# Kernel optimization log

Hardware: AMD Instinct MI355X
Metric: run time of the kernel (lower is better)

Reference implementation:

```python
import jax, jax.numpy as jnp
import numpy as np

B, S, D, H = 32, 577, 768, 12
d = D // H  # dim per head
MLP = 4 * D
EPS = 1e-5


def setup_inputs() -> dict:
    key = jax.random.key(0)
    ks = jax.random.split(key, 6)
    sc = 0.02
    return {
        "x": jax.random.normal(ks[0], (B, S, D), jnp.float32),
        "ln1_g": jnp.ones((D,), jnp.float32),
        "ln1_b": jnp.zeros((D,), jnp.float32),
        "Wq": jax.random.normal(ks[1], (H, d, d), jnp.float32) * sc,
        "bq": jnp.zeros((H, d), jnp.float32),
        "Wk": jax.random.normal(ks[2], (H, d, d), jnp.float32) * sc,
        "bk": jnp.zeros((H, d), jnp.float32),
        "Wv": jax.random.normal(ks[3], (H, d, d), jnp.float32) * sc,
        "bv": jnp.zeros((H, d), jnp.float32),
        "ln2_g": jnp.ones((D,), jnp.float32),
        "ln2_b": jnp.zeros((D,), jnp.float32),
        "W1": jax.random.normal(ks[4], (D, MLP), jnp.float32) * sc,
        "b1": jnp.zeros((MLP,), jnp.float32),
        "W2": jax.random.normal(ks[5], (MLP, D), jnp.float32) * sc,
        "b2": jnp.zeros((D,), jnp.float32),
    }


def layer_norm(x, g, b):
    mu = jnp.mean(x, axis=-1, keepdims=True)
    var = jnp.mean(jnp.square(x - mu), axis=-1, keepdims=True)
    return (x - mu) * jax.lax.rsqrt(var + EPS) * g + b


def msa(x, Wq, bq, Wk, bk, Wv, bv):
    # x: [B,S,D]; each head only sees its own slice of the hidden dim.
    xh = x.reshape(B, S, H, d)
    q = jnp.einsum("bshd,hde->bshe", xh, Wq) + bq
    k = jnp.einsum("bshd,hde->bshe", xh, Wk) + bk
    v = jnp.einsum("bshd,hde->bshe", xh, Wv) + bv
    scores = jnp.einsum("bqhe,bkhe->bhqk", q, k) / jnp.sqrt(jnp.float32(d))
    attn = jax.nn.softmax(scores, axis=-1)  # [B,H,S,S]
    out = jnp.einsum("bhqk,bkhe->bqhe", attn, v)
    return out.reshape(B, S, D)  # head-wise hstack == reshape


def reference(x, ln1_g, ln1_b, Wq, bq, Wk, bk, Wv, bv, ln2_g, ln2_b, W1, b1, W2, b2):
    out = x + msa(layer_norm(x, ln1_g, ln1_b), Wq, bq, Wk, bk, Wv, bv)
    h = layer_norm(out, ln2_g, ln2_b)
    mlp = jax.nn.gelu(h @ W1 + b1, approximate=False) @ W2 + b2
    return out + mlp
```

## Files before the change

kernel.cpp:

```cpp
#include <hip/hip_runtime.h>
#include <hip/hip_bf16.h>


#define kB   32
#define kS   577
#define kD   768
#define kH   12
#define kd   64
#define kMLP 3072
#define kTOK (kB * kS)
#define kMPAD 18688

typedef short short8 __attribute__((ext_vector_type(8)));
typedef short short4v __attribute__((ext_vector_type(4)));
typedef float f32x4 __attribute__((ext_vector_type(4)));
typedef float f32x16 __attribute__((ext_vector_type(16)));
typedef unsigned u32x4 __attribute__((ext_vector_type(4)));
typedef __bf16 bf16x8 __attribute__((ext_vector_type(8)));

__device__ inline short f2bf(float f) {
  unsigned u = __float_as_uint(f);
  unsigned r = (u + 0x7FFFu + ((u >> 16) & 1u)) >> 16;
  return (short)r;
}

__device__ inline f32x4 mfma16(short8 a, short8 b, f32x4 c) {
  return __builtin_amdgcn_mfma_f32_16x16x32_bf16(
      __builtin_bit_cast(bf16x8, a), __builtin_bit_cast(bf16x8, b), c, 0, 0, 0);
}

__device__ inline f32x16 mfma32(short8 a, short8 b, f32x16 c) {
  return __builtin_amdgcn_mfma_f32_32x32x16_bf16(
      __builtin_bit_cast(bf16x8, a), __builtin_bit_cast(bf16x8, b), c, 0, 0, 0);
}

__device__ inline void load_lds16(const short* g, short* l) {
  __builtin_amdgcn_global_load_lds(
      (__attribute__((address_space(1))) void*)(g),
      (__attribute__((address_space(3))) void*)(l), 16, 0, 0);
}

__device__ inline unsigned cvtpk(float lo, float hi) {
  unsigned r;
  asm("v_cvt_pk_bf16_f32 %0, %1, %2" : "=v"(r) : "v"(lo), "v"(hi));
  return r;
}

__device__ inline void pl32(unsigned &a, unsigned &b) {
  typedef int int2v __attribute__((ext_vector_type(2)));
  int2v r = __builtin_amdgcn_permlane32_swap((int)a, (int)b, false, false);
  a = (unsigned)r[0];
  b = (unsigned)r[1];
}

__device__ inline float gelu_f(float x) {
  float u = x * x;
  float z = x * fmaf(0.0713548162f, u, 1.5957691216f);
  float e = __expf(z);
  return x - x / (e + 1.0f);
}

__global__ __launch_bounds__(256) void ln_kernel(const float* __restrict__ x,
                                                 const float* __restrict__ g,
                                                 const float* __restrict__ b,
                                                 short* __restrict__ out) {
  int row = blockIdx.x;
  const float* xr = x + (size_t)row * kD;
  int t = threadIdx.x;
  float v0 = xr[t], v1 = xr[t + 256], v2 = xr[t + 512];
  float s = v0 + v1 + v2;
  float ss = v0 * v0 + v1 * v1 + v2 * v2;
#pragma unroll
  for (int off = 1; off < 64; off <<= 1) {
    s += __shfl_xor(s, off, 64);
    ss += __shfl_xor(ss, off, 64);
  }
  __shared__ float red[8];
  int wid = t >> 6;
  if ((t & 63) == 0) { red[wid * 2] = s; red[wid * 2 + 1] = ss; }
  __syncthreads();
  s = red[0] + red[2] + red[4] + red[6];
  ss = red[1] + red[3] + red[5] + red[7];
  float mean = s * (1.f / kD);
  float var = ss * (1.f / kD) - mean * mean;
  float rstd = rsqrtf(var + 1e-5f);
  size_t o = (size_t)row * kD;
  out[o + t]       = f2bf((v0 - mean) * rstd * g[t]       + b[t]);
  out[o + t + 256] = f2bf((v1 - mean) * rstd * g[t + 256] + b[t + 256]);
  out[o + t + 512] = f2bf((v2 - mean) * rstd * g[t + 512] + b[t + 512]);
}

__global__ __launch_bounds__(256) void transpose_bf16(const float* __restrict__ in,
                                                      short* __restrict__ out,
                                                      int R, int C) {
  __shared__ short tile[64][66];
  int c0 = blockIdx.x * 64, r0 = blockIdx.y * 64;
  int t = threadIdx.x;
  int c = t & 63, rr = t >> 6;
#pragma unroll
  for (int p = 0; p < 16; p++) {
    int r = p * 4 + rr;
    tile[r][c] = f2bf(in[(size_t)(r0 + r) * C + c0 + c]);
  }
  __syncthreads();
  int r2 = t & 63, cc = t >> 6;
#pragma unroll
  for (int p = 0; p < 16; p++) {
    int c2 = p * 4 + cc;
    out[(size_t)(c0 + c2) * R + r0 + r2] = tile[r2][c2];
  }
}

__global__ void pack_qkv(const float* __restrict__ Wq, const float* __restrict__ Wk,
                         const float* __restrict__ Wv, short* __restrict__ out) {
  int idx = blockIdx.x * 256 + threadIdx.x;
  if (idx >= kH * 192 * kd) return;
  int h = idx / (192 * kd);
  int j = (idx / kd) % 192;
  int k = idx % kd;
  int m = j >> 6, e = j & 63;
  const float* W = (m == 0) ? Wq : (m == 1) ? Wk : Wv;
  out[idx] = f2bf(W[((size_t)h * kd + k) * kd + e]);
}

__global__ __launch_bounds__(192) void qkv_gemm(const short* __restrict__ xn,
                                                const short* __restrict__ wt,
                                                const float* __restrict__ bq,
                                                const float* __restrict__ bk,
                                                const float* __restrict__ bv,
                                                short* __restrict__ Qb,
                                                short* __restrict__ Kb,
                                                short* __restrict__ Vb) {
  int t0 = blockIdx.x * 64;
  int h = blockIdx.y;
  __shared__ __align__(16) short As[64][72];
  __shared__ __align__(16) short Bs[192][72];
  int tid = threadIdx.x;
  for (int c = tid; c < 64 * 8; c += 192) {
    int row = c >> 3, c8 = c & 7;
    short8 v = {};
    int tok = t0 + row;
    if (tok < kTOK) v = *(const short8*)(xn + (size_t)tok * kD + h * kd + c8 * 8);
    *(short8*)&As[row][c8 * 8] = v;
  }
  const short* wth = wt + (size_t)h * 192 * kd;
  for (int c = tid; c < 192 * 8; c += 192) {
    int row = c >> 3, c8 = c & 7;
    *(short8*)&Bs[row][c8 * 8] = *(const short8*)(wth + row * kd + c8 * 8);
  }
  __syncthreads();
  int w = tid >> 6, l = tid & 63, l15 = l & 15, l4 = l >> 4;
  f32x4 acc[4][4] = {};
  short8 aF[4][2], bF[4][2];
#pragma unroll
  for (int rf = 0; rf < 4; rf++)
#pragma unroll
    for (int kk = 0; kk < 2; kk++)
      aF[rf][kk] = *(const short8*)&As[16 * rf + l15][32 * kk + 8 * l4];
#pragma unroll
  for (int cf = 0; cf < 4; cf++)
#pragma unroll
    for (int kk = 0; kk < 2; kk++)
      bF[cf][kk] = *(const short8*)&Bs[w * 64 + 16 * cf + l15][32 * kk + 8 * l4];
#pragma unroll
  for (int rf = 0; rf < 4; rf++)
#pragma unroll
    for (int cf = 0; cf < 4; cf++) {
      f32x4 c = acc[rf][cf];
      c = mfma16(aF[rf][0], bF[cf][0], c);
      c = mfma16(aF[rf][1], bF[cf][1], c);
      acc[rf][cf] = c;
    }
  const float* bias = (w == 0) ? bq : (w == 1) ? bk : bv;
  short* Out = (w == 0) ? Qb : (w == 1) ? Kb : Vb;
  float scale = (w == 0) ? 0.125f : 1.0f;
#pragma unroll
  for (int rf = 0; rf < 4; rf++) {
    int rowb = 16 * rf + 4 * l4;
#pragma unroll
    for (int cf = 0; cf < 4; cf++) {
      int col = 16 * cf + l15;
      float bs = bias[h * kd + col];
#pragma unroll
      for (int r = 0; r < 4; r++) {
        int tok = t0 + rowb + r;
        if (tok >= kTOK) continue;
        int bb = tok / kS, ssi = tok % kS;
        Out[(((size_t)bb * kH + h) * kS + ssi) * kd + col] =
            f2bf((acc[rf][cf][r] + bs) * scale);
      }
    }
  }
}

__global__ __launch_bounds__(256) void attn_kernel(const short* __restrict__ Qb,
                                                   const short* __restrict__ Kb,
                                                   const short* __restrict__ Vb,
                                                   const float* __restrict__ x,
                                                   float* __restrict__ out) {
  int qt = blockIdx.x, h = blockIdx.y, b = blockIdx.z;
  const size_t baseHS = ((size_t)b * kH + h) * kS;
  __shared__ __align__(16) short Klds[2][64 * 64];
  __shared__ __align__(16) short Vlds[2][64 * 64];
  int tid = threadIdx.x;
  int w = tid >> 6, l = tid & 63;
  int l31 = l & 31, hi = l >> 5;
  int q0w = qt * 128 + w * 32;
  bool active = (q0w < kS);

  int qg = q0w + l31;
  const short* qp = Qb + (baseHS + (qg > 576 ? 576 : qg)) * kd + 8 * hi;
  short8 qf[4];
#pragma unroll
  for (int ks = 0; ks < 4; ks++) qf[ks] = *(const short8*)(qp + 16 * ks);

  auto stageK = [&](int kbase, short* dst) {
#pragma unroll
    for (int c = 0; c < 2; c++) {
      int chunk = tid + 256 * c;
      int row = chunk >> 3, sl = chunk & 7;
      int sr = kbase + row; if (sr > 576) sr = 576;
      load_lds16(Kb + (baseHS + sr) * kd + 8 * (sl ^ (row & 7)),
                 dst + (chunk & ~63) * 8);
    }
  };
  short4v vr0[2], vr1[2];
  auto stageV_load = [&](int kbase) {
#pragma unroll
    for (int c = 0; c < 2; c++) {
      int task = tid + 256 * c;
      int vp = task >> 4, vc = task & 15;
      int r0 = kbase + 2 * vp;     if (r0 > 576) r0 = 576;
      int r1 = kbase + 2 * vp + 1; if (r1 > 576) r1 = 576;
      vr0[c] = *(const short4v*)(Vb + (baseHS + r0) * kd + 4 * vc);
      vr1[c] = *(const short4v*)(Vb + (baseHS + r1) * kd + 4 * vc);
    }
  };
  auto stageV_write = [&](short* dst) {
#pragma unroll
    for (int c = 0; c < 2; c++) {
      int task = tid + 256 * c;
      int vp = task >> 4, vc = task & 15;
      int kv2 = 2 * vp;
#pragma unroll
      for (int j = 0; j < 4; j++) {
        int d = 4 * vc + j;
        *(unsigned*)((char*)dst + d * 128 + ((kv2 * 2) ^ ((d & 7) << 4))) =
            (unsigned)(unsigned short)vr0[c][j] |
            ((unsigned)(unsigned short)vr1[c][j] << 16);
      }
    }
  };

  stageK(0, Klds[0]);
  stageV_load(0);
  stageV_write(Vlds[0]);
  __syncthreads();

  f32x16 o0 = {}, o1 = {};
  float m_run = -1e30f, l_run = 0.f;
  int cur = 0;
  const int NT = 10;

  for (int kt = 0; kt < NT; kt++) {
    int kbase = kt * 64;
    bool has_next = (kt + 1 < NT);
    if (has_next) {
      stageK(kbase + 64, Klds[cur ^ 1]);
      stageV_load(kbase + 64);
    }
    u32x4 pa[4];
    if (active) {
      const char* Kc = (const char*)Klds[cur];
      f32x16 st0 = {}, st1 = {};
      __builtin_amdgcn_s_setprio(1);
#pragma unroll
      for (int ks = 0; ks < 4; ks++) {
        int xr = ((2 * ks + hi) ^ (l31 & 7)) << 4;
        short8 k0 = *(const short8*)(Kc + l31 * 128 + xr);
        short8 k1 = *(const short8*)(Kc + (32 + l31) * 128 + xr);
        st0 = mfma32(k0, qf[ks], st0);
        st1 = mfma32(k1, qf[ks], st1);
      }
      __builtin_amdgcn_s_setprio(0);
      if (kbase + 64 > kS) {
#pragma unroll
        for (int r = 0; r < 16; r++) {
          int cr = (r & 3) + 8 * (r >> 2) + 4 * hi;
          if (kbase + cr > 576)      st0[r] = -1e30f;
          if (kbase + 32 + cr > 576) st1[r] = -1e30f;
        }
      }
      float mx = st0[0];
#pragma unroll
      for (int r = 0; r < 16; r++) {
        mx = fmaxf(mx, st0[r]);
        mx = fmaxf(mx, st1[r]);
      }
      mx = fmaxf(mx, __shfl_xor(mx, 32, 64));
      bool need = !__all(mx <= m_run + 8.0f);
      if (need) {
        float mnew = fmaxf(m_run, mx);
        float al = __expf(m_run - mnew);
        m_run = mnew;
        l_run *= al;
#pragma unroll
        for (int r = 0; r < 16; r++) {
          int cr = (r & 3) + 8 * (r >> 2) + 4 * hi;
          float ar = __shfl(al, cr, 64);
          o0[r] *= ar;
          o1[r] *= ar;
        }
      }
      float rs = 0.f;
#pragma unroll
      for (int r = 0; r < 16; r++) {
        float p0 = __expf(st0[r] - m_run); st0[r] = p0;
        float p1 = __expf(st1[r] - m_run); st1[r] = p1;
        rs += p0 + p1;
      }
      rs += __shfl_xor(rs, 32, 64);
      l_run += rs;
      {
        unsigned a0 = cvtpk(st0[0], st0[1]),   b0 = cvtpk(st0[4], st0[5]);   pl32(a0, b0);
        unsigned a1 = cvtpk(st0[2], st0[3]),   b1 = cvtpk(st0[6], st0[7]);   pl32(a1, b1);
        pa[0] = (u32x4){a0, a1, b0, b1};
        unsigned c0 = cvtpk(st0[8], st0[9]),   d0 = cvtpk(st0[12], st0[13]); pl32(c0, d0);
        unsigned c1 = cvtpk(st0[10], st0[11]), d1 = cvtpk(st0[14], st0[15]); pl32(c1, d1);
        pa[1] = (u32x4){c0, c1, d0, d1};
        unsigned e0 = cvtpk(st1[0], st1[1]),   f0 = cvtpk(st1[4], st1[5]);   pl32(e0, f0);
        unsigned e1 = cvtpk(st1[2], st1[3]),   f1 = cvtpk(st1[6], st1[7]);   pl32(e1, f1);
        pa[2] = (u32x4){e0, e1, f0, f1};
        unsigned g0 = cvtpk(st1[8], st1[9]),   h0 = cvtpk(st1[12], st1[13]); pl32(g0, h0);
        unsigned g1 = cvtpk(st1[10], st1[11]), h1 = cvtpk(st1[14], st1[15]); pl32(g1, h1);
        pa[3] = (u32x4){g0, g1, h0, h1};
      }
      const char* Vc = (const char*)Vlds[cur];
      __builtin_amdgcn_s_setprio(1);
#pragma unroll
      for (int ks = 0; ks < 4; ks++) {
        int xr = ((2 * ks + hi) ^ (l31 & 7)) << 4;
        short8 v0 = *(const short8*)(Vc + l31 * 128 + xr);
        short8 v1 = *(const short8*)(Vc + (32 + l31) * 128 + xr);
        o0 = mfma32(__builtin_bit_cast(short8, pa[ks]), v0, o0);
        o1 = mfma32(__builtin_bit_cast(short8, pa[ks]), v1, o1);
      }
      __builtin_amdgcn_s_setprio(0);
    }
    if (has_next) stageV_write(Vlds[cur ^ 1]);
    __syncthreads();
    cur ^= 1;
  }

  if (active) {
#pragma unroll
    for (int r = 0; r < 16; r++) {
      int cr = (r & 3) + 8 * (r >> 2) + 4 * hi;
      int qq = q0w + cr;
      if (qq < kS) {
        float lq = __shfl(l_run, cr, 64);
        float rl = 1.0f / lq;
        size_t gi = ((size_t)b * kS + qq) * kD + h * kd + l31;
        out[gi]      = x[gi]      + o0[r] * rl;
        out[gi + 32] = x[gi + 32] + o1[r] * rl;
      } else {
        (void)__shfl(l_run, cr, 64);
      }
    }
  }
}

__global__ __launch_bounds__(512, 4) void gemm_bb(const short* __restrict__ A,
                                                  const short* __restrict__ BT,
                                                  const float* __restrict__ bias,
                                                  short* __restrict__ outb,
                                                  float* __restrict__ outf,
                                                  int M, int N, int K, int mode) {
  __shared__ __align__(16) short As[256 * 64];
  __shared__ __align__(16) short Bs[128 * 64];

  int nwg = gridDim.x, bid = blockIdx.x;
  int q = nwg >> 3, r = nwg & 7;
  int xcd = bid & 7, lx = bid >> 3;
  int swz = (xcd < r ? xcd * (q + 1) : r * (q + 1) + (xcd - r) * q) + lx;
  int gn = N >> 7;
  int nt = swz % gn, mt = swz / gn;
  int m0 = mt << 8, n0 = nt << 7;

  int tid = threadIdx.x;
  int w = tid >> 6, l = tid & 63, l15 = l & 15, l4 = l >> 4;
  int wm = w >> 1, wn = w & 1;

  int srow = tid >> 3;
  int sslot = (tid & 7) ^ (srow & 7);
  int sdst = (tid & ~63) * 8;
  const short* Asrc = A + (size_t)(m0 + srow) * K + sslot * 8;
  const short* Bsrc = BT + (size_t)(n0 + srow) * K + sslot * 8;

  const char* ldsA = (const char*)As + wm * 8192;
  const char* ldsB = (const char*)Bs + wn * 8192;

  f32x4 acc[4][4] = {};

  for (int k0 = 0; k0 < K; k0 += 64) {
    __syncthreads();
#pragma unroll
    for (int i = 0; i < 4; i++)
      load_lds16(Asrc + (size_t)(64 * i) * K + k0, As + i * 4096 + sdst);
#pragma unroll
    for (int j = 0; j < 2; j++)
      load_lds16(Bsrc + (size_t)(64 * j) * K + k0, Bs + j * 4096 + sdst);
    __syncthreads();
#pragma unroll
    for (int kk = 0; kk < 2; kk++) {
      short8 aF[4], bF[4];
#pragma unroll
      for (int i = 0; i < 4; i++) {
        int ra = 16 * i + l15;
        aF[i] = *(const short8*)(ldsA + ra * 128 + (((kk * 4 + l4) ^ (ra & 7)) << 4));
        bF[i] = *(const short8*)(ldsB + ra * 128 + (((kk * 4 + l4) ^ (ra & 7)) << 4));
      }
#pragma unroll
      for (int i = 0; i < 4; i++)
#pragma unroll
        for (int j = 0; j < 4; j++)
          acc[i][j] = mfma16(aF[i], bF[j], acc[i][j]);
    }
  }

#pragma unroll
  for (int i = 0; i < 4; i++) {
#pragma unroll
    for (int j = 0; j < 4; j++) {
      int col = n0 + wn * 64 + 16 * j + l15;
      float bs = bias[col];
#pragma unroll
      for (int rr = 0; rr < 4; rr++) {
        int row = m0 + wm * 64 + 16 * i + 4 * l4 + rr;
        if (row >= M) continue;
        float v = acc[i][j][rr] + bs;
        if (mode == 0) {
          outb[(size_t)row * N + col] = f2bf(gelu_f(v));
        } else {
          outf[(size_t)row * N + col] += v;
        }
      }
    }
  }
}

extern "C" void kernel_launch(void* const* d_in, const int* in_sizes, int n_in,
                              void* d_out, int out_size, void* d_ws, size_t ws_size,
                              hipStream_t stream) {
  const float* x     = (const float*)d_in[0];
  const float* ln1_g = (const float*)d_in[1];
  const float* ln1_b = (const float*)d_in[2];
  const float* Wq    = (const float*)d_in[3];
  const float* bq    = (const float*)d_in[4];
  const float* Wk    = (const float*)d_in[5];
  const float* bk    = (const float*)d_in[6];
  const float* Wv    = (const float*)d_in[7];
  const float* bv    = (const float*)d_in[8];
  const float* ln2_g = (const float*)d_in[9];
  const float* ln2_b = (const float*)d_in[10];
  const float* W1    = (const float*)d_in[11];
  const float* b1    = (const float*)d_in[12];
  const float* W2    = (const float*)d_in[13];
  const float* b2    = (const float*)d_in[14];
  float* out = (float*)d_out;

  char* ws = (char*)d_ws;
  size_t off = 0;
  auto alloc = [&](size_t bytes) {
    size_t o = off;
    off += (bytes + 255) & ~(size_t)255;
    return o;
  };
  short* xn    = (short*)(ws + alloc((size_t)kTOK * kD * 2));
  short* wqkvT = (short*)(ws + alloc((size_t)kH * 192 * kd * 2));
  short* w1T   = (short*)(ws + alloc((size_t)kMLP * kD * 2));
  short* w2T   = (short*)(ws + alloc((size_t)kD * kMLP * 2));
  short* Qb    = (short*)(ws + alloc((size_t)kTOK * kD * 2));
  short* Kb    = (short*)(ws + alloc((size_t)kTOK * kD * 2));
  short* Vb    = (short*)(ws + alloc((size_t)kTOK * kD * 2));
  short* hbuf  = (short*)(ws + alloc((size_t)kMPAD * kD * 2));
  short* gbuf  = (short*)(ws + alloc((size_t)kMPAD * kMLP * 2));

  ln_kernel<<<kTOK, 256, 0, stream>>>(x, ln1_g, ln1_b, xn);
  transpose_bf16<<<dim3(kMLP / 64, kD / 64), 256, 0, stream>>>(W1, w1T, kD, kMLP);
  transpose_bf16<<<dim3(kD / 64, kMLP / 64), 256, 0, stream>>>(W2, w2T, kMLP, kD);
  pack_qkv<<<(kH * 192 * kd + 255) / 256, 256, 0, stream>>>(Wq, Wk, Wv, wqkvT);
  qkv_gemm<<<dim3((kTOK + 63) / 64, kH), 192, 0, stream>>>(xn, wqkvT, bq, bk, bv, Qb, Kb, Vb);
  attn_kernel<<<dim3(5, kH, kB), 256, 0, stream>>>(Qb, Kb, Vb, x, out);
  ln_kernel<<<kTOK, 256, 0, stream>>>(out, ln2_g, ln2_b, hbuf);
  gemm_bb<<<(kMPAD / 256) * (kMLP / 128), 512, 0, stream>>>(
      hbuf, w1T, b1, gbuf, nullptr, kTOK, kMLP, kD, 0);
  gemm_bb<<<(kMPAD / 256) * (kD / 128), 512, 0, stream>>>(
      gbuf, w2T, b2, nullptr, out, kTOK, kD, kMLP, 1);
}
```

Before: 469.6 us.

## Use dedicated 128x128-tile GEMM with XCD swizzle for MLP down-projection

Adds a new GEMM kernel with 128x128 tiles, 256 threads and an XCD-aware block remapping, and uses it for the second MLP matmul (K=3072, N=768) instead of the generic 256x128 kernel. The smaller tiles double the block count for this narrow-N GEMM to improve CU utilisation and wave balance. In exchange, each tile reuses data less and the main loop is single-buffered with two barriers per k-step.

New measurement: 468.0 us. About the same (-0.3%).

```diff
diff --git a/kernel.cpp b/kernel.cpp
--- a/kernel.cpp
+++ b/kernel.cpp
@@ -449,6 +449,79 @@
   }
 }
 
+__global__ __launch_bounds__(256, 4) void gemm2b(const short* __restrict__ A,
+                                                 const short* __restrict__ BT,
+                                                 const float* __restrict__ bias,
+                                                 float* __restrict__ outf,
+                                                 int M, int N, int K) {
+  __shared__ __align__(16) short As[128 * 64];
+  __shared__ __align__(16) short Bs[128 * 64];
+
+  int nwg = gridDim.x, bid = blockIdx.x;
+  int q = nwg >> 3, r = nwg & 7;
+  int xcd = bid & 7, lx = bid >> 3;
+  int swz = (xcd < r ? xcd * (q + 1) : r * (q + 1) + (xcd - r) * q) + lx;
+  int gn = N >> 7;
+  int nt = swz % gn, mt = swz / gn;
+  int m0 = mt << 7, n0 = nt << 7;
+
+  int tid = threadIdx.x;
+  int w = tid >> 6, l = tid & 63, l15 = l & 15, l4 = l >> 4;
+  int wm = w >> 1, wn = w & 1;
+
+  int srow = tid >> 3;
+  int sslot = (tid & 7) ^ (srow & 7);
+  int sdst = (tid & ~63) * 8;
+  const short* Asrc = A + (size_t)(m0 + srow) * K + sslot * 8;
+  const short* Bsrc = BT + (size_t)(n0 + srow) * K + sslot * 8;
+
+  const char* ldsA = (const char*)As + wm * 8192;
+  const char* ldsB = (const char*)Bs + wn * 8192;
+
+  f32x4 acc[4][4] = {};
+
+  for (int k0 = 0; k0 < K; k0 += 64) {
+    __syncthreads();
+#pragma unroll
+    for (int i = 0; i < 4; i++)
+      load_lds16(Asrc + (size_t)(32 * i) * K + k0, As + i * 2048 + sdst);
+#pragma unroll
+    for (int j = 0; j < 4; j++)
+      load_lds16(Bsrc + (size_t)(32 * j) * K + k0, Bs + j * 2048 + sdst);
+    __syncthreads();
+#pragma unroll
+    for (int kk = 0; kk < 2; kk++) {
+      short8 aF[4], bF[4];
+#pragma unroll
+      for (int i = 0; i < 4; i++) {
+        int ra = 16 * i + l15;
+        aF[i] = *(const short8*)(ldsA + ra * 128 + (((kk * 4 + l4) ^ (ra & 7)) << 4));
+        bF[i] = *(const short8*)(ldsB + ra * 128 + (((kk * 4 + l4) ^ (ra & 7)) << 4));
+      }
+#pragma unroll
+      for (int i = 0; i < 4; i++)
+#pragma unroll
+        for (int j = 0; j < 4; j++)
+          acc[i][j] = mfma16(aF[i], bF[j], acc[i][j]);
+    }
+  }
+
+#pragma unroll
+  for (int i = 0; i < 4; i++) {
+#pragma unroll
+    for (int j = 0; j < 4; j++) {
+      int col = n0 + wn * 64 + 16 * j + l15;
+      float bs = bias[col];
+#pragma unroll
+      for (int rr = 0; rr < 4; rr++) {
+        int row = m0 + wm * 64 + 16 * i + 4 * l4 + rr;
+        if (row >= M) continue;
+        outf[(size_t)row * N + col] += acc[i][j][rr] + bs;
+      }
+    }
+  }
+}
+
 extern "C" void kernel_launch(void* const* d_in, const int* in_sizes, int n_in,
                               void* d_out, int out_size, void* d_ws, size_t ws_size,
                               hipStream_t stream) {
@@ -495,6 +568,6 @@
   ln_kernel<<<kTOK, 256, 0, stream>>>(out, ln2_g, ln2_b, hbuf);
   gemm_bb<<<(kMPAD / 256) * (kMLP / 128), 512, 0, stream>>>(
       hbuf, w1T, b1, gbuf, nullptr, kTOK, kMLP, kD, 0);
-  gemm_bb<<<(kMPAD / 256) * (kD / 128), 512, 0, stream>>>(
-      gbuf, w2T, b2, nullptr, out, kTOK, kD, kMLP, 1);
-}
+  gemm2b<<<(kMPAD / 128) * (kD / 128), 256, 0, stream>>>(
+      gbuf, w2T, b2, out, kTOK, kD, kMLP);
+}
```
